# Optimization experiments

Measured on AMD Instinct MI355X. Metric: run time of the kernel, lower is better.

Reference implementation:

```python
import jax, jax.numpy as jnp
import numpy as np

B, N, C = 256, 2048, 64      # batch(residues), num_queries/keys(extra MSA seqs), channels
H, KD, VD, OD = 8, 8, 8, 64  # heads, per-head key dim, per-head value dim, output dim


def setup_inputs() -> dict:
    key = jax.random.key(0)
    ks = jax.random.split(key, 9)
    q_data = jax.random.normal(ks[0], (B, N, C), dtype=jnp.float32)
    m_data = jax.random.normal(ks[1], (B, N, C), dtype=jnp.float32)
    # per-sequence 0/1 mask, broadcast across the channel dim (same rank as q_data)
    seq_mask = (jax.random.uniform(ks[2], (B, N, 1)) < 0.9).astype(jnp.float32)
    q_mask = jnp.broadcast_to(seq_mask, (B, N, C))
    bias = jnp.zeros((B, 1, N), dtype=jnp.float32)  # ignored by forward (AF2 quirk)
    q_weights = jax.random.normal(ks[3], (C, H, KD), dtype=jnp.float32) * 0.05
    k_weights = jax.random.normal(ks[4], (C, KD), dtype=jnp.float32) * 0.05
    v_weights = jax.random.normal(ks[5], (C, VD), dtype=jnp.float32) * 0.05
    o_weights = jax.random.normal(ks[6], (H, VD, OD), dtype=jnp.float32) * 0.05
    o_bias = jnp.zeros((OD,), dtype=jnp.float32)
    gating_w = jax.random.normal(ks[7], (C, H, VD), dtype=jnp.float32) * 0.05
    gating_b = jnp.ones((H, VD), dtype=jnp.float32)
    return {
        "q_data": q_data, "m_data": m_data, "q_mask": q_mask, "bias": bias,
        "q_weights": q_weights, "k_weights": k_weights, "v_weights": v_weights,
        "o_weights": o_weights, "o_bias": o_bias,
        "gating_w": gating_w, "gating_b": gating_b,
    }


def reference(q_data, m_data, q_mask, bias, q_weights, k_weights, v_weights,
              o_weights, o_bias, gating_w, gating_b):
    # v, k projections: [B,N,C] x [C,d] -> [B,N,d]
    v = jnp.einsum('bka,ac->bkc', m_data, v_weights)
    k = jnp.einsum('bka,ac->bkc', m_data, k_weights)
    # masked mean over the query axis (dim 1); mask has full channel dim -> factor 1
    q_avg = jnp.sum(q_mask * q_data, axis=1) / (jnp.sum(q_mask, axis=1) + 1e-10)
    # pooled query: [B,C] x [C,H,KD] -> [B,H,KD], scaled by 1/sqrt(per-head key dim)
    q = jnp.einsum('ba,ahc->bhc', q_avg, q_weights) * (KD ** (-0.5))
    # attention bias from mask (the `bias` argument is overwritten, as in the original)
    mask_bias = 1e9 * (q_mask[:, None, :, 0] - 1.0)              # [B,1,N]
    logits = jnp.einsum('bhc,bkc->bhk', q, k) + mask_bias        # [B,H,N]
    weights = jax.nn.softmax(logits, axis=-1)
    weighted_avg = jnp.einsum('bhk,bkc->bhc', weights, v)        # [B,H,VD]
    # sigmoid gating per query
    gate = jax.nn.sigmoid(jnp.einsum('bqc,chv->bqhv', q_data, gating_w) + gating_b)
    gated = weighted_avg[:, None] * gate                          # [B,N,H,VD]
    out = jnp.einsum('bqhc,hco->bqo', gated, o_weights) + o_bias  # [B,N,OD]
    return out
```

## Files before the change

### kernel.cpp

```cpp
#include <hip/hip_runtime.h>
#include <hip/hip_bf16.h>
#include <math.h>

#define BN 256
#define NN 2048
#define CC 64

#define WS_SUMQ 0
#define WS_SUMM (WS_SUMQ + BN * 2 * 64)
#define WS_V    (WS_SUMM + BN * 2)
#define WS_S    (WS_V + BN * 2 * 64)
#define WS_MASK (WS_S + BN * 2 * 8)

typedef __bf16 bf16x8 __attribute__((ext_vector_type(8)));
typedef float f32x4 __attribute__((ext_vector_type(4)));

__global__ __launch_bounds__(1024, 8) void k_pool(const float* __restrict__ qd,
                                                  const float* __restrict__ qm,
                                                  float* __restrict__ ws) {
    const int b = blockIdx.x >> 1, bh = blockIdx.x & 1;
    const int tid = threadIdx.x;
    const int row0 = bh * 1024;

    __shared__ float smask[1024];
    __shared__ float wsum[16];
    __shared__ float red[64][64];

    const float m0 = qm[((size_t)b * NN + row0 + tid) * CC];
    smask[tid] = m0;
    ws[WS_MASK + (size_t)b * NN + row0 + tid] = m0;
    float msum = m0;
    for (int off = 32; off > 0; off >>= 1) msum += __shfl_down(msum, off, 64);
    if ((tid & 63) == 0) wsum[tid >> 6] = msum;
    __syncthreads();

    const float4* qb4 = (const float4*)(qd + ((size_t)b * NN + row0) * CC);
    const int rbase = tid >> 4;
    float4 acc = {0.f, 0.f, 0.f, 0.f};
#pragma unroll
    for (int half = 0; half < 2; ++half) {
        float4 v[8];
#pragma unroll
        for (int j = 0; j < 8; ++j)
            v[j] = qb4[(size_t)(half * 8 + j) * 1024 + tid];
#pragma unroll
        for (int j = 0; j < 8; ++j) {
            const float m = smask[(half * 8 + j) * 64 + rbase];
            acc.x += m * v[j].x; acc.y += m * v[j].y;
            acc.z += m * v[j].z; acc.w += m * v[j].w;
        }
    }
    *(float4*)&red[rbase][(tid & 15) * 4] = acc;
    __syncthreads();
    if (tid < 64) {
        float s = 0.f;
#pragma unroll
        for (int g = 0; g < 64; ++g) s += red[g][tid];
        ws[WS_SUMQ + (size_t)(b * 2 + bh) * 64 + tid] = s;
    }
    if (tid == 0) {
        float s = 0.f;
#pragma unroll
        for (int g = 0; g < 16; ++g) s += wsum[g];
        ws[WS_SUMM + b * 2 + bh] = s;
    }
}

__global__ __launch_bounds__(1024) void k_attn(const float* __restrict__ md,
                                               const float* __restrict__ qw,
                                               const float* __restrict__ kw,
                                               const float* __restrict__ vw,
                                               float* __restrict__ ws) {
    const int b = blockIdx.x >> 1, nhalf = blockIdx.x & 1;
    const int tid = threadIdx.x;

    __shared__ float qa[64], ql[64];
    __shared__ float wkv[64][16];
    __shared__ float PV[1024][17];
    __shared__ float partV[16][64];
    __shared__ float partS[16][8];

    const int n = nhalf * 1024 + tid;
    const float* rowp = md + ((size_t)b * NN + n) * CC;
    const float mk = ws[WS_MASK + (size_t)b * NN + n];
    float4 buf[8];
#pragma unroll
    for (int j = 0; j < 8; ++j) buf[j] = ((const float4*)rowp)[j];

    if (tid < 64) {
        const float s = ws[WS_SUMQ + (size_t)(b * 2 + 0) * 64 + tid] +
                        ws[WS_SUMQ + (size_t)(b * 2 + 1) * 64 + tid];
        const float den = ws[WS_SUMM + b * 2 + 0] + ws[WS_SUMM + b * 2 + 1];
        qa[tid] = s / (den + 1e-10f);
    }
    __syncthreads();
    if (tid < 64) {
        float s = 0.f;
#pragma unroll
        for (int c = 0; c < 64; ++c) s += qa[c] * qw[c * 64 + tid];
        ql[tid] = s * 0.35355339059327373f;
    }
    __syncthreads();
    if (tid < 512) {
        const int c = tid >> 3, h = tid & 7;
        float s = 0.f;
#pragma unroll
        for (int d = 0; d < 8; ++d) s += kw[c * 8 + d] * ql[h * 8 + d];
        wkv[c][h] = s;
        wkv[c][8 + h] = vw[tid];
    }
    __syncthreads();

    float la[8], va[8];
#pragma unroll
    for (int h = 0; h < 8; ++h) { la[h] = 0.f; va[h] = 0.f; }
#pragma unroll
    for (int hv = 0; hv < 2; ++hv) {
        if (hv == 1) {
#pragma unroll
            for (int j = 0; j < 8; ++j) buf[j] = ((const float4*)rowp)[8 + j];
        }
#pragma unroll
        for (int j = 0; j < 8; ++j) {
            const float xa[4] = {buf[j].x, buf[j].y, buf[j].z, buf[j].w};
#pragma unroll
            for (int q = 0; q < 4; ++q) {
                const int c = hv * 32 + j * 4 + q;
                const float4* wr = (const float4*)wkv[c];
                const float4 wa = wr[0], wb = wr[1], wc = wr[2], wd = wr[3];
                const float x = xa[q];
                la[0] += x * wa.x; la[1] += x * wa.y; la[2] += x * wa.z; la[3] += x * wa.w;
                la[4] += x * wb.x; la[5] += x * wb.y; la[6] += x * wb.z; la[7] += x * wb.w;
                va[0] += x * wc.x; va[1] += x * wc.y; va[2] += x * wc.z; va[3] += x * wc.w;
                va[4] += x * wd.x; va[5] += x * wd.y; va[6] += x * wd.z; va[7] += x * wd.w;
            }
        }
    }

#pragma unroll
    for (int h = 0; h < 8; ++h) PV[tid][h] = mk * __expf(la[h]);
#pragma unroll
    for (int d = 0; d < 8; ++d) PV[tid][8 + d] = va[d];
    __syncthreads();

    const int w = tid >> 6, lane = tid & 63, h = lane >> 3, d = lane & 7;
    float acc = 0.f, sacc = 0.f;
    for (int i = 0; i < 64; ++i) {
        const int rr = w * 64 + i;
        const float p = PV[rr][h];
        acc += p * PV[rr][8 + d];
        sacc += p;
    }
    partV[w][lane] = acc;
    if (d == 0) partS[w][h] = sacc;
    __syncthreads();
    if (tid < 64) {
        float s = 0.f;
#pragma unroll
        for (int g = 0; g < 16; ++g) s += partV[g][tid];
        ws[WS_V + (size_t)(b * 2 + nhalf) * 64 + tid] = s;
    }
    if (tid < 8) {
        float s = 0.f;
#pragma unroll
        for (int g = 0; g < 16; ++g) s += partS[g][tid];
        ws[WS_S + (size_t)(b * 2 + nhalf) * 8 + tid] = s;
    }
}

__global__ __launch_bounds__(256) void k_out(const float* __restrict__ qd,
                                             const float* __restrict__ ow,
                                             const float* __restrict__ obias,
                                             const float* __restrict__ gw,
                                             const float* __restrict__ gb,
                                             const float* __restrict__ ws,
                                             float* __restrict__ out) {
    const int b = blockIdx.x >> 3, chunk = blockIdx.x & 7;
    const int tid = threadIdx.x;
    const int w = tid >> 6, lane = tid & 63, q16 = lane >> 4, c16 = lane & 15;

    __shared__ float s_wavg[64], s_sden[8];
    if (tid < 64) {
        s_wavg[tid] = ws[WS_V + (size_t)(b * 2 + 0) * 64 + tid] +
                      ws[WS_V + (size_t)(b * 2 + 1) * 64 + tid];
    }
    if (tid >= 64 && tid < 72) {
        const int hh = tid - 64;
        s_sden[hh] = ws[WS_S + (size_t)(b * 2 + 0) * 8 + hh] +
                     ws[WS_S + (size_t)(b * 2 + 1) * 8 + hh];
    }
    __syncthreads();

    bf16x8 gwf[2][4], w2f[2][4];
    float gbv[4], obv[4];
#pragma unroll
    for (int kc = 0; kc < 2; ++kc) {
        const int k0 = kc * 32 + q16 * 8;
        const float inv_s = 1.f / s_sden[k0 >> 3];
#pragma unroll
        for (int t = 0; t < 4; ++t) {
            const int n2 = t * 16 + c16;
            bf16x8 gf, wf;
#pragma unroll
            for (int j = 0; j < 8; ++j) {
                gf[j] = (__bf16)gw[(size_t)(k0 + j) * 64 + n2];
                wf[j] = (__bf16)(s_wavg[k0 + j] * inv_s *
                                 ow[(size_t)(k0 + j) * 64 + n2]);
            }
            gwf[kc][t] = gf;
            w2f[kc][t] = wf;
        }
    }
#pragma unroll
    for (int t = 0; t < 4; ++t) {
        gbv[t] = gb[t * 16 + c16];
        obv[t] = obias[t * 16 + c16];
    }

    __shared__ __align__(16) __bf16 gl[4][16][72];

    const size_t base_row = (size_t)b * NN + chunk * 256 + w * 16;

    float4 cur0, cur1, cur2, cur3, nxt0, nxt1, nxt2, nxt3;
    {
        const float* arow = qd + (base_row + c16) * CC;
        cur0 = *(const float4*)(arow + q16 * 8);
        cur1 = *(const float4*)(arow + q16 * 8 + 4);
        cur2 = *(const float4*)(arow + 32 + q16 * 8);
        cur3 = *(const float4*)(arow + 32 + q16 * 8 + 4);
    }

    for (int s = 0; s < 4; ++s) {
        if (s < 3) {
            const float* arow = qd + (base_row + (s + 1) * 64 + c16) * CC;
            nxt0 = *(const float4*)(arow + q16 * 8);
            nxt1 = *(const float4*)(arow + q16 * 8 + 4);
            nxt2 = *(const float4*)(arow + 32 + q16 * 8);
            nxt3 = *(const float4*)(arow + 32 + q16 * 8 + 4);
        }
        bf16x8 af[2];
        {
            bf16x8 a;
            a[0] = (__bf16)cur0.x; a[1] = (__bf16)cur0.y; a[2] = (__bf16)cur0.z; a[3] = (__bf16)cur0.w;
            a[4] = (__bf16)cur1.x; a[5] = (__bf16)cur1.y; a[6] = (__bf16)cur1.z; a[7] = (__bf16)cur1.w;
            af[0] = a;
            a[0] = (__bf16)cur2.x; a[1] = (__bf16)cur2.y; a[2] = (__bf16)cur2.z; a[3] = (__bf16)cur2.w;
            a[4] = (__bf16)cur3.x; a[5] = (__bf16)cur3.y; a[6] = (__bf16)cur3.z; a[7] = (__bf16)cur3.w;
            af[1] = a;
        }
        f32x4 accg[4] = {{0.f, 0.f, 0.f, 0.f}, {0.f, 0.f, 0.f, 0.f},
                         {0.f, 0.f, 0.f, 0.f}, {0.f, 0.f, 0.f, 0.f}};
#pragma unroll
        for (int kc = 0; kc < 2; ++kc)
#pragma unroll
            for (int t = 0; t < 4; ++t)
                accg[t] = __builtin_amdgcn_mfma_f32_16x16x32_bf16(af[kc], gwf[kc][t],
                                                                  accg[t], 0, 0, 0);
#pragma unroll
        for (int t = 0; t < 4; ++t)
#pragma unroll
            for (int r2 = 0; r2 < 4; ++r2) {
                const float x = accg[t][r2] + gbv[t];
                const float g = 1.f / (1.f + __expf(-x));
                gl[w][q16 * 4 + r2][t * 16 + c16] = (__bf16)g;
            }
        __asm__ volatile("s_waitcnt lgkmcnt(0)" ::: "memory");
        bf16x8 a2[2];
#pragma unroll
        for (int kc = 0; kc < 2; ++kc)
            a2[kc] = *(const bf16x8*)&gl[w][c16][kc * 32 + q16 * 8];
        f32x4 acco[4] = {{0.f, 0.f, 0.f, 0.f}, {0.f, 0.f, 0.f, 0.f},
                         {0.f, 0.f, 0.f, 0.f}, {0.f, 0.f, 0.f, 0.f}};
#pragma unroll
        for (int kc = 0; kc < 2; ++kc)
#pragma unroll
            for (int t = 0; t < 4; ++t)
                acco[t] = __builtin_amdgcn_mfma_f32_16x16x32_bf16(a2[kc], w2f[kc][t],
                                                                  acco[t], 0, 0, 0);
        __asm__ volatile("s_waitcnt lgkmcnt(0)" ::: "memory");
        float* orow = out + (base_row + s * 64) * CC;
#pragma unroll
        for (int t = 0; t < 4; ++t)
#pragma unroll
            for (int r2 = 0; r2 < 4; ++r2)
                orow[(size_t)(q16 * 4 + r2) * 64 + t * 16 + c16] = acco[t][r2] + obv[t];
        cur0 = nxt0; cur1 = nxt1; cur2 = nxt2; cur3 = nxt3;
    }
}

extern "C" void kernel_launch(void* const* d_in, const int* in_sizes, int n_in,
                              void* d_out, int out_size, void* d_ws, size_t ws_size,
                              hipStream_t stream) {
    const float* q_data = (const float*)d_in[0];
    const float* m_data = (const float*)d_in[1];
    const float* q_mask = (const float*)d_in[2];
    const float* q_w = (const float*)d_in[4];
    const float* k_w = (const float*)d_in[5];
    const float* v_w = (const float*)d_in[6];
    const float* o_w = (const float*)d_in[7];
    const float* o_b = (const float*)d_in[8];
    const float* g_w = (const float*)d_in[9];
    const float* g_b = (const float*)d_in[10];
    float* out = (float*)d_out;
    float* ws = (float*)d_ws;

    hipLaunchKernelGGL(k_pool, dim3(BN * 2), dim3(1024), 0, stream, q_data, q_mask, ws);
    hipLaunchKernelGGL(k_attn, dim3(BN * 2), dim3(1024), 0, stream, m_data, q_w, k_w,
                       v_w, ws);
    hipLaunchKernelGGL(k_out, dim3(BN * 8), dim3(256), 0, stream, q_data, o_w, o_b,
                       g_w, g_b, ws, out);
}
```

Baseline: 453.3 us.

## Fuse pooling, attention and gated output into one per-batch kernel

```diff
diff --git a/kernel.cpp b/kernel.cpp
--- a/kernel.cpp
+++ b/kernel.cpp
@@ -6,91 +6,62 @@
 #define NN 2048
 #define CC 64
 
-#define WS_SUMQ 0
-#define WS_SUMM (WS_SUMQ + BN * 2 * 64)
-#define WS_V    (WS_SUMM + BN * 2)
-#define WS_S    (WS_V + BN * 2 * 64)
-#define WS_MASK (WS_S + BN * 2 * 8)
-
 typedef __bf16 bf16x8 __attribute__((ext_vector_type(8)));
 typedef float f32x4 __attribute__((ext_vector_type(4)));
 
-__global__ __launch_bounds__(1024, 8) void k_pool(const float* __restrict__ qd,
-                                                  const float* __restrict__ qm,
-                                                  float* __restrict__ ws) {
-    const int b = blockIdx.x >> 1, bh = blockIdx.x & 1;
+__global__ __launch_bounds__(1024, 4) void k_fused(
+    const float* __restrict__ qd, const float* __restrict__ md,
+    const float* __restrict__ qm, const float* __restrict__ qw,
+    const float* __restrict__ kw, const float* __restrict__ vw,
+    const float* __restrict__ ow, const float* __restrict__ obias,
+    const float* __restrict__ gw, const float* __restrict__ gb,
+    float* __restrict__ out) {
+    const int b = blockIdx.x;
     const int tid = threadIdx.x;
-    const int row0 = bh * 1024;
-
-    __shared__ float smask[1024];
-    __shared__ float wsum[16];
-    __shared__ float red[64][64];
-
-    const float m0 = qm[((size_t)b * NN + row0 + tid) * CC];
-    smask[tid] = m0;
-    ws[WS_MASK + (size_t)b * NN + row0 + tid] = m0;
-    float msum = m0;
-    for (int off = 32; off > 0; off >>= 1) msum += __shfl_down(msum, off, 64);
-    if ((tid & 63) == 0) wsum[tid >> 6] = msum;
-    __syncthreads();
-
-    const float4* qb4 = (const float4*)(qd + ((size_t)b * NN + row0) * CC);
-    const int rbase = tid >> 4;
-    float4 acc = {0.f, 0.f, 0.f, 0.f};
-#pragma unroll
-    for (int half = 0; half < 2; ++half) {
-        float4 v[8];
-#pragma unroll
-        for (int j = 0; j < 8; ++j)
-            v[j] = qb4[(size_t)(half * 8 + j) * 1024 + tid];
-#pragma unroll
-        for (int j = 0; j < 8; ++j) {
-            const float m = smask[(half * 8 + j) * 64 + rbase];
-            acc.x += m * v[j].x; acc.y += m * v[j].y;
-            acc.z += m * v[j].z; acc.w += m * v[j].w;
-        }
-    }
-    *(float4*)&red[rbase][(tid & 15) * 4] = acc;
-    __syncthreads();
-    if (tid < 64) {
-        float s = 0.f;
-#pragma unroll
-        for (int g = 0; g < 64; ++g) s += red[g][tid];
-        ws[WS_SUMQ + (size_t)(b * 2 + bh) * 64 + tid] = s;
-    }
-    if (tid == 0) {
-        float s = 0.f;
-#pragma unroll
-        for (int g = 0; g < 16; ++g) s += wsum[g];
-        ws[WS_SUMM + b * 2 + bh] = s;
-    }
-}
-
-__global__ __launch_bounds__(1024) void k_attn(const float* __restrict__ md,
-                                               const float* __restrict__ qw,
-                                               const float* __restrict__ kw,
-                                               const float* __restrict__ vw,
-                                               float* __restrict__ ws) {
-    const int b = blockIdx.x >> 1, nhalf = blockIdx.x & 1;
-    const int tid = threadIdx.x;
-
-    __shared__ float qa[64], ql[64];
+
+    __shared__ float smask[2048];
+    __shared__ __align__(16) float PVpool[1024 * 17];
     __shared__ float wkv[64][16];
-    __shared__ float PV[1024][17];
     __shared__ float partV[16][64];
     __shared__ float partS[16][8];
-
-    const int n = nhalf * 1024 + tid;
-    const float* rowp = md + ((size_t)b * NN + n) * CC;
-    const float mk = ws[WS_MASK + (size_t)b * NN + n];
-    float4 buf[8];
-#pragma unroll
-    for (int j = 0; j < 8; ++j) buf[j] = ((const float4*)rowp)[j];
+    __shared__ float qa[64], ql[64];
+    __shared__ float s_wavg[64], s_sden[8];
+    __shared__ __align__(16) __bf16 gwT[4096];
+    __shared__ __align__(16) __bf16 w2T[4096];
+
+#define PVF(n, j) PVpool[(n) * 17 + (j)]
+#define RED(g, c) PVpool[(g) * 64 + (c)]
+
+    smask[tid] = qm[((size_t)b * NN + tid) * CC];
+    smask[tid + 1024] = qm[((size_t)b * NN + tid + 1024) * CC];
+    __syncthreads();
+
+    {
+        const float4* qb4 = (const float4*)(qd + (size_t)b * NN * CC);
+        const int rbase = tid >> 4;
+        float4 acc = {0.f, 0.f, 0.f, 0.f};
+        for (int g4 = 0; g4 < 4; ++g4) {
+            float4 v[8];
+#pragma unroll
+            for (int j = 0; j < 8; ++j)
+                v[j] = qb4[(size_t)(g4 * 8 + j) * 1024 + tid];
+#pragma unroll
+            for (int j = 0; j < 8; ++j) {
+                const float m = smask[(g4 * 8 + j) * 64 + rbase];
+                acc.x += m * v[j].x; acc.y += m * v[j].y;
+                acc.z += m * v[j].z; acc.w += m * v[j].w;
+            }
+        }
+        *(float4*)&RED(rbase, (tid & 15) * 4) = acc;
+    }
+    __syncthreads();
 
     if (tid < 64) {
-        const float s = ws[WS_SUMQ + (size_t)(b * 2 + 0) * 64 + tid] +
-                        ws[WS_SUMQ + (size_t)(b * 2 + 1) * 64 + tid];
-        const float den = ws[WS_SUMM + b * 2 + 0] + ws[WS_SUMM + b * 2 + 1];
+        float den = 0.f;
+        for (int g = 0; g < 32; ++g) den += smask[tid + g * 64];
+        for (int off = 1; off < 64; off <<= 1) den += __shfl_xor(den, off, 64);
+        float s = 0.f;
+        for (int g = 0; g < 64; ++g) s += RED(g, tid);
         qa[tid] = s / (den + 1e-10f);
     }
     __syncthreads();
@@ -111,115 +82,95 @@
     }
     __syncthreads();
 
-    float la[8], va[8];
-#pragma unroll
-    for (int h = 0; h < 8; ++h) { la[h] = 0.f; va[h] = 0.f; }
-#pragma unroll
-    for (int hv = 0; hv < 2; ++hv) {
-        if (hv == 1) {
-#pragma unroll
-            for (int j = 0; j < 8; ++j) buf[j] = ((const float4*)rowp)[8 + j];
-        }
-#pragma unroll
-        for (int j = 0; j < 8; ++j) {
-            const float xa[4] = {buf[j].x, buf[j].y, buf[j].z, buf[j].w};
-#pragma unroll
-            for (int q = 0; q < 4; ++q) {
-                const int c = hv * 32 + j * 4 + q;
-                const float4* wr = (const float4*)wkv[c];
-                const float4 wa = wr[0], wb = wr[1], wc = wr[2], wd = wr[3];
-                const float x = xa[q];
-                la[0] += x * wa.x; la[1] += x * wa.y; la[2] += x * wa.z; la[3] += x * wa.w;
-                la[4] += x * wb.x; la[5] += x * wb.y; la[6] += x * wb.z; la[7] += x * wb.w;
-                va[0] += x * wc.x; va[1] += x * wc.y; va[2] += x * wc.z; va[3] += x * wc.w;
-                va[4] += x * wd.x; va[5] += x * wd.y; va[6] += x * wd.z; va[7] += x * wd.w;
-            }
-        }
-    }
-
-#pragma unroll
-    for (int h = 0; h < 8; ++h) PV[tid][h] = mk * __expf(la[h]);
-#pragma unroll
-    for (int d = 0; d < 8; ++d) PV[tid][8 + d] = va[d];
-    __syncthreads();
-
-    const int w = tid >> 6, lane = tid & 63, h = lane >> 3, d = lane & 7;
-    float acc = 0.f, sacc = 0.f;
-    for (int i = 0; i < 64; ++i) {
-        const int rr = w * 64 + i;
-        const float p = PV[rr][h];
-        acc += p * PV[rr][8 + d];
-        sacc += p;
-    }
-    partV[w][lane] = acc;
-    if (d == 0) partS[w][h] = sacc;
-    __syncthreads();
-    if (tid < 64) {
-        float s = 0.f;
-#pragma unroll
-        for (int g = 0; g < 16; ++g) s += partV[g][tid];
-        ws[WS_V + (size_t)(b * 2 + nhalf) * 64 + tid] = s;
-    }
-    if (tid < 8) {
-        float s = 0.f;
-#pragma unroll
-        for (int g = 0; g < 16; ++g) s += partS[g][tid];
-        ws[WS_S + (size_t)(b * 2 + nhalf) * 8 + tid] = s;
-    }
-}
-
-__global__ __launch_bounds__(256) void k_out(const float* __restrict__ qd,
-                                             const float* __restrict__ ow,
-                                             const float* __restrict__ obias,
-                                             const float* __restrict__ gw,
-                                             const float* __restrict__ gb,
-                                             const float* __restrict__ ws,
-                                             float* __restrict__ out) {
-    const int b = blockIdx.x >> 3, chunk = blockIdx.x & 7;
-    const int tid = threadIdx.x;
+    float vreg = 0.f, sreg = 0.f;
+    for (int pass = 0; pass < 2; ++pass) {
+        const int row = pass * 1024 + tid;
+        const float mk = smask[row];
+        const float4* rowp4 = (const float4*)(md + ((size_t)b * NN + row) * CC);
+        float la[8], va[8];
+#pragma unroll
+        for (int h = 0; h < 8; ++h) { la[h] = 0.f; va[h] = 0.f; }
+#pragma unroll
+        for (int hv = 0; hv < 2; ++hv) {
+            float4 buf[8];
+#pragma unroll
+            for (int j = 0; j < 8; ++j) buf[j] = rowp4[hv * 8 + j];
+#pragma unroll
+            for (int j = 0; j < 8; ++j) {
+                const float xa[4] = {buf[j].x, buf[j].y, buf[j].z, buf[j].w};
+#pragma unroll
+                for (int q = 0; q < 4; ++q) {
+                    const int c = hv * 32 + j * 4 + q;
+                    const float4* wr = (const float4*)wkv[c];
+                    const float4 wa = wr[0], wb = wr[1], wc = wr[2], wd = wr[3];
+                    const float x = xa[q];
+                    la[0] += x * wa.x; la[1] += x * wa.y; la[2] += x * wa.z; la[3] += x * wa.w;
+                    la[4] += x * wb.x; la[5] += x * wb.y; la[6] += x * wb.z; la[7] += x * wb.w;
+                    va[0] += x * wc.x; va[1] += x * wc.y; va[2] += x * wc.z; va[3] += x * wc.w;
+                    va[4] += x * wd.x; va[5] += x * wd.y; va[6] += x * wd.z; va[7] += x * wd.w;
+                }
+            }
+        }
+#pragma unroll
+        for (int h = 0; h < 8; ++h) PVF(tid, h) = mk * __expf(la[h]);
+#pragma unroll
+        for (int d = 0; d < 8; ++d) PVF(tid, 8 + d) = va[d];
+        __syncthreads();
+        {
+            const int w = tid >> 6, lane = tid & 63, h = lane >> 3, d = lane & 7;
+            float a2 = 0.f, s2 = 0.f;
+            for (int i = 0; i < 64; ++i) {
+                const int rr = w * 64 + i;
+                const float p = PVF(rr, h);
+                a2 += p * PVF(rr, 8 + d);
+                s2 += p;
+            }
+            partV[w][lane] = a2;
+            if (d == 0) partS[w][h] = s2;
+        }
+        __syncthreads();
+        if (tid < 64) {
+            float s = 0.f;
+#pragma unroll
+            for (int g = 0; g < 16; ++g) s += partV[g][tid];
+            vreg += s;
+        }
+        if (tid < 8) {
+            float s = 0.f;
+#pragma unroll
+            for (int g = 0; g < 16; ++g) s += partS[g][tid];
+            sreg += s;
+        }
+        __syncthreads();
+    }
+    if (tid < 64) s_wavg[tid] = vreg;
+    if (tid < 8) s_sden[tid] = sreg;
+    __syncthreads();
+
+    {
+        const int k = tid >> 4;
+        const int n0 = (tid & 15) * 4;
+        const float wv = s_wavg[k] / s_sden[k >> 3];
+#pragma unroll
+        for (int u = 0; u < 4; ++u) {
+            const int n = n0 + u;
+            const int idx = n * 64 + ((((k >> 3) ^ (n & 7))) << 3) + (k & 7);
+            gwT[idx] = (__bf16)gw[(size_t)k * 64 + n];
+            w2T[idx] = (__bf16)(wv * ow[(size_t)k * 64 + n]);
+        }
+    }
     const int w = tid >> 6, lane = tid & 63, q16 = lane >> 4, c16 = lane & 15;
-
-    __shared__ float s_wavg[64], s_sden[8];
-    if (tid < 64) {
-        s_wavg[tid] = ws[WS_V + (size_t)(b * 2 + 0) * 64 + tid] +
-                      ws[WS_V + (size_t)(b * 2 + 1) * 64 + tid];
-    }
-    if (tid >= 64 && tid < 72) {
-        const int hh = tid - 64;
-        s_sden[hh] = ws[WS_S + (size_t)(b * 2 + 0) * 8 + hh] +
-                     ws[WS_S + (size_t)(b * 2 + 1) * 8 + hh];
-    }
-    __syncthreads();
-
-    bf16x8 gwf[2][4], w2f[2][4];
     float gbv[4], obv[4];
-#pragma unroll
-    for (int kc = 0; kc < 2; ++kc) {
-        const int k0 = kc * 32 + q16 * 8;
-        const float inv_s = 1.f / s_sden[k0 >> 3];
-#pragma unroll
-        for (int t = 0; t < 4; ++t) {
-            const int n2 = t * 16 + c16;
-            bf16x8 gf, wf;
-#pragma unroll
-            for (int j = 0; j < 8; ++j) {
-                gf[j] = (__bf16)gw[(size_t)(k0 + j) * 64 + n2];
-                wf[j] = (__bf16)(s_wavg[k0 + j] * inv_s *
-                                 ow[(size_t)(k0 + j) * 64 + n2]);
-            }
-            gwf[kc][t] = gf;
-            w2f[kc][t] = wf;
-        }
-    }
 #pragma unroll
     for (int t = 0; t < 4; ++t) {
         gbv[t] = gb[t * 16 + c16];
         obv[t] = obias[t * 16 + c16];
     }
-
-    __shared__ __align__(16) __bf16 gl[4][16][72];
-
-    const size_t base_row = (size_t)b * NN + chunk * 256 + w * 16;
+    __syncthreads();
+
+    __bf16* gl = (__bf16*)PVpool;
+#define GL(wv, r, c) gl[(((wv)*16 + (r)) * 72) + (c)]
+    const size_t base_row = (size_t)b * NN + (size_t)w * 128;
 
     float4 cur0, cur1, cur2, cur3, nxt0, nxt1, nxt2, nxt3;
     {
@@ -230,9 +181,9 @@
         cur3 = *(const float4*)(arow + 32 + q16 * 8 + 4);
     }
 
-    for (int s = 0; s < 4; ++s) {
-        if (s < 3) {
-            const float* arow = qd + (base_row + (s + 1) * 64 + c16) * CC;
+    for (int s = 0; s < 8; ++s) {
+        if (s < 7) {
+            const float* arow = qd + (base_row + (s + 1) * 16 + c16) * CC;
             nxt0 = *(const float4*)(arow + q16 * 8);
             nxt1 = *(const float4*)(arow + q16 * 8 + 4);
             nxt2 = *(const float4*)(arow + 32 + q16 * 8);
@@ -251,34 +202,48 @@
         f32x4 accg[4] = {{0.f, 0.f, 0.f, 0.f}, {0.f, 0.f, 0.f, 0.f},
                          {0.f, 0.f, 0.f, 0.f}, {0.f, 0.f, 0.f, 0.f}};
 #pragma unroll
-        for (int kc = 0; kc < 2; ++kc)
+        for (int kc = 0; kc < 2; ++kc) {
+            bf16x8 bf[4];
+#pragma unroll
+            for (int t = 0; t < 4; ++t) {
+                const int n = t * 16 + c16;
+                bf[t] = *(const bf16x8*)&gwT[n * 64 + (((kc * 4 + q16) ^ (n & 7)) << 3)];
+            }
 #pragma unroll
             for (int t = 0; t < 4; ++t)
-                accg[t] = __builtin_amdgcn_mfma_f32_16x16x32_bf16(af[kc], gwf[kc][t],
+                accg[t] = __builtin_amdgcn_mfma_f32_16x16x32_bf16(af[kc], bf[t],
                                                                   accg[t], 0, 0, 0);
+        }
 #pragma unroll
         for (int t = 0; t < 4; ++t)
 #pragma unroll
             for (int r2 = 0; r2 < 4; ++r2) {
                 const float x = accg[t][r2] + gbv[t];
                 const float g = 1.f / (1.f + __expf(-x));
-                gl[w][q16 * 4 + r2][t * 16 + c16] = (__bf16)g;
+                GL(w, q16 * 4 + r2, t * 16 + c16) = (__bf16)g;
             }
         __asm__ volatile("s_waitcnt lgkmcnt(0)" ::: "memory");
         bf16x8 a2[2];
 #pragma unroll
         for (int kc = 0; kc < 2; ++kc)
-            a2[kc] = *(const bf16x8*)&gl[w][c16][kc * 32 + q16 * 8];
+            a2[kc] = *(const bf16x8*)&GL(w, c16, kc * 32 + q16 * 8);
         f32x4 acco[4] = {{0.f, 0.f, 0.f, 0.f}, {0.f, 0.f, 0.f, 0.f},
                          {0.f, 0.f, 0.f, 0.f}, {0.f, 0.f, 0.f, 0.f}};
 #pragma unroll
-        for (int kc = 0; kc < 2; ++kc)
+        for (int kc = 0; kc < 2; ++kc) {
+            bf16x8 bf[4];
+#pragma unroll
+            for (int t = 0; t < 4; ++t) {
+                const int n = t * 16 + c16;
+                bf[t] = *(const bf16x8*)&w2T[n * 64 + (((kc * 4 + q16) ^ (n & 7)) << 3)];
+            }
 #pragma unroll
             for (int t = 0; t < 4; ++t)
-                acco[t] = __builtin_amdgcn_mfma_f32_16x16x32_bf16(a2[kc], w2f[kc][t],
+                acco[t] = __builtin_amdgcn_mfma_f32_16x16x32_bf16(a2[kc], bf[t],
                                                                   acco[t], 0, 0, 0);
+        }
         __asm__ volatile("s_waitcnt lgkmcnt(0)" ::: "memory");
-        float* orow = out + (base_row + s * 64) * CC;
+        float* orow = out + (base_row + s * 16) * CC;
 #pragma unroll
         for (int t = 0; t < 4; ++t)
 #pragma unroll
@@ -286,6 +251,9 @@
                 orow[(size_t)(q16 * 4 + r2) * 64 + t * 16 + c16] = acco[t][r2] + obv[t];
         cur0 = nxt0; cur1 = nxt1; cur2 = nxt2; cur3 = nxt3;
     }
+#undef GL
+#undef PVF
+#undef RED
 }
 
 extern "C" void kernel_launch(void* const* d_in, const int* in_sizes, int n_in,
@@ -302,11 +270,8 @@
     const float* g_w = (const float*)d_in[9];
     const float* g_b = (const float*)d_in[10];
     float* out = (float*)d_out;
-    float* ws = (float*)d_ws;
-
-    hipLaunchKernelGGL(k_pool, dim3(BN * 2), dim3(1024), 0, stream, q_data, q_mask, ws);
-    hipLaunchKernelGGL(k_attn, dim3(BN * 2), dim3(1024), 0, stream, m_data, q_w, k_w,
-                       v_w, ws);
-    hipLaunchKernelGGL(k_out, dim3(BN * 8), dim3(256), 0, stream, q_data, o_w, o_b,
-                       g_w, g_b, ws, out);
+    (void)d_ws; (void)ws_size; (void)in_sizes; (void)n_in; (void)out_size;
+
+    hipLaunchKernelGGL(k_fused, dim3(BN), dim3(1024), 0, stream, q_data, m_data,
+                       q_mask, q_w, k_w, v_w, o_w, o_b, g_w, g_b, out);
 }
```

Result: faster. 437.1 us (-3.6%).
